# Kernel tuning notes

Measured on AMD Instinct MI355X. Metric: run time of the kernel, lower is better.

Reference implementation:

```python
import jax, jax.numpy as jnp
import numpy as np

B, A, D = 64, 4096, 512
TOP_K = 5

def setup_inputs() -> dict:
    key = jax.random.key(0)
    k1, k2, k3 = jax.random.split(key, 3)
    s_embed = jax.random.normal(k1, (B, D), dtype=jnp.float32)
    a_embeds = jax.random.normal(k2, (B, A, D), dtype=jnp.float32)
    available_mask = jax.random.randint(k3, (B, A), 0, 2) > 0
    # make sure each row has at least one available action
    available_mask = available_mask.at[:, 0].set(True)
    return {"s_embed": s_embed, "a_embeds": a_embeds,
            "available_mask": available_mask, "alpha": 1}


def reference(s_embed, a_embeds, available_mask, alpha):
    alpha = jnp.float32(alpha)
    # logits[b,a] = <s_embed[b], a_embeds[b,a]>
    logits = jnp.einsum('bd,bad->ba', s_embed, a_embeds)  # [B, A]
    # masked_fill unavailable actions with (global min - 1)
    fill = jnp.min(logits) - 1.0
    logits = jnp.where(available_mask, logits, fill)
    # top-k mask via scatter
    k = min(logits.shape[1], TOP_K)
    _, top_ids = jax.lax.top_k(logits, k)  # [B, k]
    rows = jnp.arange(logits.shape[0])[:, None]
    top_mask = jnp.zeros(logits.shape, dtype=bool).at[rows, top_ids].set(True)
    # temperature softmax (max-shifted, matching the torch code)
    probs = jax.nn.softmax((logits - jnp.max(logits, -1, keepdims=True)) / alpha, axis=-1)
    # keep only available & top-k, renormalize
    keep = available_mask & top_mask
    probs = jnp.where(keep, probs, 0.0)
    probs = probs / jnp.sum(probs, -1, keepdims=True)
    # categorical sample (zeros -> -inf logits, never sampled)
    action = jax.random.categorical(jax.random.key(42), jnp.log(probs), axis=-1)
    return action, logits
```

## Files before the change

### kernel.cpp

```cpp
#include <hip/hip_runtime.h>
#include <cstdint>
#include <cstddef>

#define NB 64
#define NA 4096
#define ND 512

__device__ __forceinline__ unsigned rotl32(unsigned x, int d){ return (x << d) | (x >> (32 - d)); }

__device__ unsigned threefry_bits(unsigned n){
  const unsigned ks0 = 0u;
  const unsigned ks1 = 42u;
  const unsigned ks2 = 0x1BD11BDAu ^ ks0 ^ ks1;
  unsigned x0 = 0u;
  unsigned x1 = n;
  x0 += ks0; x1 += ks1;
  const int r0[4] = {13, 15, 26, 6};
  const int r1[4] = {17, 29, 16, 24};
  #pragma unroll
  for (int j = 0; j < 4; j++){ x0 += x1; x1 = rotl32(x1, r0[j]); x1 ^= x0; }
  x0 += ks1; x1 += ks2 + 1u;
  #pragma unroll
  for (int j = 0; j < 4; j++){ x0 += x1; x1 = rotl32(x1, r1[j]); x1 ^= x0; }
  x0 += ks2; x1 += ks0 + 2u;
  #pragma unroll
  for (int j = 0; j < 4; j++){ x0 += x1; x1 = rotl32(x1, r0[j]); x1 ^= x0; }
  x0 += ks0; x1 += ks1 + 3u;
  #pragma unroll
  for (int j = 0; j < 4; j++){ x0 += x1; x1 = rotl32(x1, r1[j]); x1 ^= x0; }
  x0 += ks1; x1 += ks2 + 4u;
  #pragma unroll
  for (int j = 0; j < 4; j++){ x0 += x1; x1 = rotl32(x1, r0[j]); x1 ^= x0; }
  x0 += ks2; x1 += ks0 + 5u;
  return x0 ^ x1;
}

__global__ __launch_bounds__(256) void dot_kernel(const float* __restrict__ s,
                                                  const float* __restrict__ ae,
                                                  float* __restrict__ logits,
                                                  float* __restrict__ minbuf){
  __shared__ float sm[4];
  int wave = threadIdx.x >> 6;
  int lane = threadIdx.x & 63;
  int blk  = blockIdx.x;
  int b     = blk >> 8;
  int abase = ((blk & 255) << 4) | (wave << 2);
  const float* sr = s + b * ND;
  float4 s0 = *(const float4*)(sr + lane * 4);
  float4 s1 = *(const float4*)(sr + 256 + lane * 4);
  const float* ar = ae + ((size_t)(b * NA) + abase) * ND + lane * 4;
  float4 a00 = *(const float4*)(ar);
  float4 a01 = *(const float4*)(ar + 256);
  float4 a10 = *(const float4*)(ar + 512);
  float4 a11 = *(const float4*)(ar + 768);
  float4 a20 = *(const float4*)(ar + 1024);
  float4 a21 = *(const float4*)(ar + 1280);
  float4 a30 = *(const float4*)(ar + 1536);
  float4 a31 = *(const float4*)(ar + 1792);
  float p0 = a00.x*s0.x + a00.y*s0.y + a00.z*s0.z + a00.w*s0.w
           + a01.x*s1.x + a01.y*s1.y + a01.z*s1.z + a01.w*s1.w;
  float p1 = a10.x*s0.x + a10.y*s0.y + a10.z*s0.z + a10.w*s0.w
           + a11.x*s1.x + a11.y*s1.y + a11.z*s1.z + a11.w*s1.w;
  float p2 = a20.x*s0.x + a20.y*s0.y + a20.z*s0.z + a20.w*s0.w
           + a21.x*s1.x + a21.y*s1.y + a21.z*s1.z + a21.w*s1.w;
  float p3 = a30.x*s0.x + a30.y*s0.y + a30.z*s0.z + a30.w*s0.w
           + a31.x*s1.x + a31.y*s1.y + a31.z*s1.z + a31.w*s1.w;
  #pragma unroll
  for (int off = 32; off > 0; off >>= 1){
    p0 += __shfl_xor(p0, off, 64);
    p1 += __shfl_xor(p1, off, 64);
    p2 += __shfl_xor(p2, off, 64);
    p3 += __shfl_xor(p3, off, 64);
  }
  if (lane == 0){
    float4 v = make_float4(p0, p1, p2, p3);
    *(float4*)(logits + (size_t)b * NA + abase) = v;
    sm[wave] = fminf(fminf(p0, p1), fminf(p2, p3));
  }
  __syncthreads();
  if (threadIdx.x == 0)
    minbuf[blk] = fminf(fminf(sm[0], sm[1]), fminf(sm[2], sm[3]));
}

__global__ __launch_bounds__(256) void row_kernel(float* __restrict__ out,
                                                  const void* __restrict__ maskp,
                                                  const float* __restrict__ minbuf,
                                                  const unsigned* __restrict__ alpha_raw){
  __shared__ float row[NA];
  __shared__ float su[4];
  __shared__ float rv[4]; __shared__ int ri[4];
  __shared__ float selv[5]; __shared__ int seli[5];
  __shared__ int s_mflag;
  __shared__ float s_fill;
  int b = blockIdx.x;
  int t = threadIdx.x;
  float* lrow = out + NB + (size_t)b * NA;
  const unsigned char* m8  = (const unsigned char*)maskp;
  const unsigned*      m32 = (const unsigned*)maskp;

  if (t == 0) s_mflag = 1;
  __syncthreads();
  for (int i = t; i < 4096; i += 256)
    if (m32[i] > 1u) s_mflag = 0;

  float e = minbuf[t];
  for (int i = t + 256; i < 16384; i += 256) e = fminf(e, minbuf[i]);
  #pragma unroll
  for (int off = 32; off > 0; off >>= 1) e = fminf(e, __shfl_xor(e, off, 64));
  if ((t & 63) == 0) su[t >> 6] = e;
  __syncthreads();
  if (t == 0)
    s_fill = fminf(fminf(su[0], su[1]), fminf(su[2], su[3])) - 1.0f;
  __syncthreads();
  int   mflag = s_mflag;
  float fill  = s_fill;

  for (int a = t; a < NA; a += 256){
    int idx = b * NA + a;
    bool av = mflag ? (m32[idx] != 0u) : (m8[idx] != 0);
    float v = lrow[a];
    float mv = av ? v : fill;
    row[a]  = mv;
    lrow[a] = mv;
  }
  __syncthreads();

  for (int k = 0; k < 5; k++){
    float bv = -INFINITY; int bi = 0x7FFFFFFF;
    for (int a = t; a < NA; a += 256){
      float v = row[a];
      if (v > bv){ bv = v; bi = a; }
    }
    #pragma unroll
    for (int off = 32; off > 0; off >>= 1){
      float ov = __shfl_xor(bv, off, 64);
      int   oi = __shfl_xor(bi, off, 64);
      if (ov > bv || (ov == bv && oi < bi)){ bv = ov; bi = oi; }
    }
    if ((t & 63) == 0){ rv[t >> 6] = bv; ri[t >> 6] = bi; }
    __syncthreads();
    if (t == 0){
      float fv = rv[0]; int fi = ri[0];
      for (int w = 1; w < 4; w++)
        if (rv[w] > fv || (rv[w] == fv && ri[w] < fi)){ fv = rv[w]; fi = ri[w]; }
      selv[k] = fv; seli[k] = fi;
      row[fi] = -INFINITY;
    }
    __syncthreads();
  }

  if (t == 0){
    unsigned ab = *alpha_raw;
    float alpha = (ab < 0x00800000u) ? (float)(int)ab : __uint_as_float(ab);
    float best = -INFINITY; int ba = 0;
    for (int k = 0; k < 5; k++){
      int idx  = seli[k];
      int gidx = b * NA + idx;
      bool av = mflag ? (m32[gidx] != 0u) : (m8[gidx] != 0);
      if (!av) continue;
      unsigned bits = threefry_bits((unsigned)gidx);
      float f = __uint_as_float((bits >> 9) | 0x3F800000u) - 1.0f;
      const float tiny = 1.17549435e-38f;
      float u = fmaxf(tiny, f + tiny);
      float g = -logf(-logf(u));
      float sc = selv[k] / alpha + g;
      if (sc > best){ best = sc; ba = idx; }
    }
    out[b] = (float)ba;
  }
}

extern "C" void kernel_launch(void* const* d_in, const int* in_sizes, int n_in,
                              void* d_out, int out_size, void* d_ws, size_t ws_size,
                              hipStream_t stream){
  const float*    s     = (const float*)d_in[0];
  const float*    ae    = (const float*)d_in[1];
  const void*     mask  = d_in[2];
  const unsigned* alpha = (const unsigned*)d_in[3];
  float* out = (float*)d_out;
  float* ws  = (float*)d_ws;

  hipLaunchKernelGGL(dot_kernel, dim3(NB * NA / 16), dim3(256), 0, stream, s, ae, out + NB, ws);
  hipLaunchKernelGGL(row_kernel, dim3(NB),           dim3(256), 0, stream, out, mask, ws, alpha);
}
```

Measured before the change: 130.7 us.

## Fuse dot and row kernels into one cooperative persistent kernel with grid sync

Merges the dot-product kernel and the per-row top-k/sampling kernel into a single cooperative launch. Persistent blocks grid-stride over one action per wave, each wave loading 512 floats, then a grid-wide sync replaces the kernel boundary. Afterwards only the first 64 blocks run the row stage. This removes one launch and the dependency gap between kernels. The cost is less memory-level parallelism per wave (two float4 loads per iteration instead of eight), a grid sync, the 16KB shared row buffer reducing occupancy, and a per-call occupancy query on the host.

After: 391.6 us. 200% more time.

```diff
diff --git a/kernel.cpp b/kernel.cpp
--- a/kernel.cpp
+++ b/kernel.cpp
@@ -1,10 +1,14 @@
 #include <hip/hip_runtime.h>
+#include <hip/hip_cooperative_groups.h>
 #include <cstdint>
 #include <cstddef>
+
+namespace cg = cooperative_groups;
 
 #define NB 64
 #define NA 4096
 #define ND 512
+#define NGROUPS (NB * NA / 4)
 
 __device__ __forceinline__ unsigned rotl32(unsigned x, int d){ return (x << d) | (x >> (32 - d)); }
 
@@ -35,66 +39,55 @@
   return x0 ^ x1;
 }
 
-__global__ __launch_bounds__(256) void dot_kernel(const float* __restrict__ s,
-                                                  const float* __restrict__ ae,
-                                                  float* __restrict__ logits,
-                                                  float* __restrict__ minbuf){
-  __shared__ float sm[4];
-  int wave = threadIdx.x >> 6;
-  int lane = threadIdx.x & 63;
-  int blk  = blockIdx.x;
-  int b     = blk >> 8;
-  int abase = ((blk & 255) << 4) | (wave << 2);
-  const float* sr = s + b * ND;
-  float4 s0 = *(const float4*)(sr + lane * 4);
-  float4 s1 = *(const float4*)(sr + 256 + lane * 4);
-  const float* ar = ae + ((size_t)(b * NA) + abase) * ND + lane * 4;
-  float4 a00 = *(const float4*)(ar);
-  float4 a01 = *(const float4*)(ar + 256);
-  float4 a10 = *(const float4*)(ar + 512);
-  float4 a11 = *(const float4*)(ar + 768);
-  float4 a20 = *(const float4*)(ar + 1024);
-  float4 a21 = *(const float4*)(ar + 1280);
-  float4 a30 = *(const float4*)(ar + 1536);
-  float4 a31 = *(const float4*)(ar + 1792);
-  float p0 = a00.x*s0.x + a00.y*s0.y + a00.z*s0.z + a00.w*s0.w
-           + a01.x*s1.x + a01.y*s1.y + a01.z*s1.z + a01.w*s1.w;
-  float p1 = a10.x*s0.x + a10.y*s0.y + a10.z*s0.z + a10.w*s0.w
-           + a11.x*s1.x + a11.y*s1.y + a11.z*s1.z + a11.w*s1.w;
-  float p2 = a20.x*s0.x + a20.y*s0.y + a20.z*s0.z + a20.w*s0.w
-           + a21.x*s1.x + a21.y*s1.y + a21.z*s1.z + a21.w*s1.w;
-  float p3 = a30.x*s0.x + a30.y*s0.y + a30.z*s0.z + a30.w*s0.w
-           + a31.x*s1.x + a31.y*s1.y + a31.z*s1.z + a31.w*s1.w;
-  #pragma unroll
-  for (int off = 32; off > 0; off >>= 1){
-    p0 += __shfl_xor(p0, off, 64);
-    p1 += __shfl_xor(p1, off, 64);
-    p2 += __shfl_xor(p2, off, 64);
-    p3 += __shfl_xor(p3, off, 64);
-  }
-  if (lane == 0){
-    float4 v = make_float4(p0, p1, p2, p3);
-    *(float4*)(logits + (size_t)b * NA + abase) = v;
-    sm[wave] = fminf(fminf(p0, p1), fminf(p2, p3));
-  }
-  __syncthreads();
-  if (threadIdx.x == 0)
-    minbuf[blk] = fminf(fminf(sm[0], sm[1]), fminf(sm[2], sm[3]));
-}
-
-__global__ __launch_bounds__(256) void row_kernel(float* __restrict__ out,
-                                                  const void* __restrict__ maskp,
-                                                  const float* __restrict__ minbuf,
-                                                  const unsigned* __restrict__ alpha_raw){
+__global__ __launch_bounds__(256, 8)
+void fused_kernel(const float* __restrict__ s,
+                  const float* __restrict__ ae,
+                  const void*  __restrict__ maskp,
+                  const unsigned* __restrict__ alpha_raw,
+                  float* __restrict__ out,
+                  float* __restrict__ minbuf){
+  __shared__ float smin[4];
   __shared__ float row[NA];
   __shared__ float su[4];
   __shared__ float rv[4]; __shared__ int ri[4];
   __shared__ float selv[5]; __shared__ int seli[5];
   __shared__ int s_mflag;
   __shared__ float s_fill;
-  int b = blockIdx.x;
-  int t = threadIdx.x;
-  float* lrow = out + NB + (size_t)b * NA;
+
+  const int bid  = blockIdx.x;
+  const int nblk = gridDim.x;
+  const int t    = threadIdx.x;
+  const int wave = t >> 6;
+  const int lane = t & 63;
+  float* logits = out + NB;
+
+  float wmin = INFINITY;
+  for (int g = bid; g < NGROUPS; g += nblk){
+    int b = g >> 10;
+    int a = ((g & 1023) << 2) | wave;
+    const float* ar = ae + ((size_t)b * NA + a) * ND;
+    const float* sr = s + b * ND;
+    float4 a0 = *(const float4*)(ar + lane * 4);
+    float4 a1 = *(const float4*)(ar + 256 + lane * 4);
+    float4 s0 = *(const float4*)(sr + lane * 4);
+    float4 s1 = *(const float4*)(sr + 256 + lane * 4);
+    float p = a0.x*s0.x + a0.y*s0.y + a0.z*s0.z + a0.w*s0.w
+            + a1.x*s1.x + a1.y*s1.y + a1.z*s1.z + a1.w*s1.w;
+    #pragma unroll
+    for (int off = 32; off > 0; off >>= 1) p += __shfl_xor(p, off, 64);
+    wmin = fminf(wmin, p);
+    if (lane == 0) logits[(size_t)b * NA + a] = p;
+  }
+  if (lane == 0) smin[wave] = wmin;
+  __syncthreads();
+  if (t == 0)
+    minbuf[bid] = fminf(fminf(smin[0], smin[1]), fminf(smin[2], smin[3]));
+
+  cg::this_grid().sync();
+
+  if (bid >= NB) return;
+  const int b = bid;
+  float* lrow = logits + (size_t)b * NA;
   const unsigned char* m8  = (const unsigned char*)maskp;
   const unsigned*      m32 = (const unsigned*)maskp;
 
@@ -103,8 +96,8 @@
   for (int i = t; i < 4096; i += 256)
     if (m32[i] > 1u) s_mflag = 0;
 
-  float e = minbuf[t];
-  for (int i = t + 256; i < 16384; i += 256) e = fminf(e, minbuf[i]);
+  float e = INFINITY;
+  for (int i = t; i < nblk; i += 256) e = fminf(e, minbuf[i]);
   #pragma unroll
   for (int off = 32; off > 0; off >>= 1) e = fminf(e, __shfl_xor(e, off, 64));
   if ((t & 63) == 0) su[t >> 6] = e;
@@ -180,6 +173,14 @@
   float* out = (float*)d_out;
   float* ws  = (float*)d_ws;
 
-  hipLaunchKernelGGL(dot_kernel, dim3(NB * NA / 16), dim3(256), 0, stream, s, ae, out + NB, ws);
-  hipLaunchKernelGGL(row_kernel, dim3(NB),           dim3(256), 0, stream, out, mask, ws, alpha);
+  int occ = 0;
+  (void)hipOccupancyMaxActiveBlocksPerMultiprocessor(&occ, (const void*)fused_kernel, 256, 0);
+  if (occ < 1) occ = 1;
+  if (occ > 8) occ = 8;
+  int grid = 256 * occ;
+
+  void* args[] = {(void*)&s, (void*)&ae, (void*)&mask, (void*)&alpha,
+                  (void*)&out, (void*)&ws};
+  (void)hipLaunchCooperativeKernel((const void*)fused_kernel, dim3(grid), dim3(256),
+                                   args, 0, stream);
 }
```
